# Kernel optimization log

Measured on AMD Instinct MI355X. Metric: run time of the kernel, lower is better.

The kernel has to match this reference:

```python
import jax, jax.numpy as jnp
import numpy as np

EMBED_DIM = 1024
NUM_HEADS = 16
HEAD_DIM = EMBED_DIM // NUM_HEADS


def setup_inputs() -> dict:
    key = jax.random.key(0)
    k_x, k_wqkv, k_bqkv, k_wo, k_bo = jax.random.split(key, 5)
    b, n = 2, 2048
    scale_in = 1.0 / np.sqrt(EMBED_DIM)
    return {
        "x": jax.random.normal(k_x, (b, n, EMBED_DIM), dtype=jnp.float32),
        "W_qkv": jax.random.normal(k_wqkv, (EMBED_DIM, 3 * EMBED_DIM), dtype=jnp.float32) * scale_in,
        "b_qkv": jnp.zeros((3 * EMBED_DIM,), dtype=jnp.float32),
        "W_out": jax.random.normal(k_wo, (EMBED_DIM, EMBED_DIM), dtype=jnp.float32) * scale_in,
        "b_out": jnp.zeros((EMBED_DIM,), dtype=jnp.float32),
    }


def _rope_rotate(t, cos, sin):
    # t: [b, h, n, hd]; cos/sin: [1, 1, n, hd//2]
    t1, t2 = jnp.split(t, 2, axis=-1)
    return jnp.concatenate([cos * t1 - sin * t2, sin * t1 + cos * t2], axis=-1)


def reference(x, W_qkv, b_qkv, W_out, b_out):
    b, n, d = x.shape
    h, hd = NUM_HEADS, HEAD_DIM

    qkv = x @ W_qkv + b_qkv                      # [b, n, 3d]
    q, k, v = jnp.split(qkv, 3, axis=-1)
    q, k, v = [t.reshape(b, n, h, hd).transpose(0, 2, 1, 3) for t in (q, k, v)]

    # RoPE tables
    hd2 = hd // 2
    theta = 10000.0 ** (-2.0 * jnp.arange(hd2, dtype=jnp.float32) / hd)
    freqs = jnp.arange(n, dtype=jnp.float32)[:, None] * theta[None, :]  # [n, hd2]
    cos = jnp.cos(freqs)[None, None]
    sin = jnp.sin(freqs)[None, None]
    q = _rope_rotate(q, cos, sin)
    k = _rope_rotate(k, cos, sin)

    scores = jnp.einsum('bhqd,bhkd->bhqk', q, k) / jnp.sqrt(jnp.float32(hd))
    attn = jax.nn.softmax(scores, axis=-1)       # [b, h, n, n]
    out = jnp.einsum('bhqk,bhkd->bhqd', attn, v)
    out = out.transpose(0, 2, 1, 3).reshape(b, n, d)
    return out @ W_out + b_out
```

## Files before the change

kernel.cpp:

```cpp
#include <hip/hip_runtime.h>
#include <hip/hip_bf16.h>
#include <math.h>

#define EMBED 1024
#define NHEAD 16
#define HD 64
#define BATCH 2
#define SEQ 2048
#define MTOT (BATCH * SEQ)
#define QKVN (3 * EMBED)

typedef __attribute__((ext_vector_type(8))) short short8;
typedef __attribute__((ext_vector_type(4))) float f32x4;

typedef __attribute__((address_space(1))) const unsigned int GUI;
typedef __attribute__((address_space(3))) unsigned int LUI;

__device__ __forceinline__ void gload_lds16(const void* src, void* dst) {
  __builtin_amdgcn_global_load_lds((GUI*)src, (LUI*)dst, 16, 0, 0);
}

__device__ __forceinline__ unsigned short f2bf(float f) {
  unsigned u = __builtin_bit_cast(unsigned, f);
  u += 0x7fffu + ((u >> 16) & 1u);
  return (unsigned short)(u >> 16);
}

__device__ __forceinline__ float bf2f(unsigned short u) {
  unsigned v = (unsigned)u << 16;
  return __builtin_bit_cast(float, v);
}

__device__ __forceinline__ unsigned cvt_pk_bf16(float lo, float hi) {
  unsigned r;
  asm("v_cvt_pk_bf16_f32 %0, %1, %2" : "=v"(r) : "v"(lo), "v"(hi));
  return r;
}

#if __has_builtin(__builtin_amdgcn_exp2f)
#define EXP2(x) __builtin_amdgcn_exp2f(x)
#else
#define EXP2(x) __builtin_exp2f(x)
#endif

#define QSCALE 0.1803368801111191f

__global__ __launch_bounds__(256) void k_prep(const float* __restrict__ x,
                                              unsigned short* __restrict__ Xb,
                                              const float* __restrict__ Wqkv,
                                              unsigned short* __restrict__ WqkvT,
                                              const float* __restrict__ Wout,
                                              unsigned short* __restrict__ WoT,
                                              float* __restrict__ cosT,
                                              float* __restrict__ sinT) {
  __shared__ float tile[32][33];
  const int bid = blockIdx.x, tid = threadIdx.x;
  if (bid < 4096) {
    int i = bid * 256 + tid;
    float4 v = reinterpret_cast<const float4*>(x)[i];
    ushort4 o;
    o.x = f2bf(v.x); o.y = f2bf(v.y); o.z = f2bf(v.z); o.w = f2bf(v.w);
    reinterpret_cast<ushort4*>(Xb)[i] = o;
  } else if (bid < 8192) {
    const float* W;
    unsigned short* WT;
    int n0, k0, Ncols;
    if (bid < 7168) {
      int idx = bid - 4096;
      W = Wqkv; WT = WqkvT; Ncols = QKVN;
      n0 = (idx % 96) * 32; k0 = (idx / 96) * 32;
    } else {
      int idx = bid - 7168;
      W = Wout; WT = WoT; Ncols = EMBED;
      n0 = (idx & 31) * 32; k0 = (idx >> 5) * 32;
    }
    const int tc = tid & 31, tr = tid >> 5;
    for (int i = 0; i < 4; i++) {
      int r = tr + i * 8;
      tile[r][tc] = W[(size_t)(k0 + r) * Ncols + n0 + tc];
    }
    __syncthreads();
    for (int i = 0; i < 4; i++) {
      int r = tr + i * 8;
      WT[(size_t)(n0 + r) * EMBED + k0 + tc] = f2bf(tile[tc][r]);
    }
  } else {
    int idx = (bid - 8192) * 256 + tid;
    if (idx < SEQ * 32) {
      int pos = idx >> 5, i = idx & 31;
      float theta = __expf((float)i * -0.28782313662425575f);
      float f = (float)pos * theta;
      cosT[idx] = cosf(f);
      sinT[idx] = sinf(f);
    }
  }
}

__device__ __forceinline__ void gemm_mainloop(const unsigned short* __restrict__ A,
                                              const unsigned short* __restrict__ Bt,
                                              unsigned short* Al, unsigned short* Bl,
                                              size_t m0, size_t n0,
                                              int tid, int l15, int g, int wm, int wn,
                                              f32x4 acc[4][4]) {
  const int w = tid >> 6;
  const int lane = tid & 63;
  const int srow = lane >> 3, slot = lane & 7;
  for (int k0 = 0; k0 < 1024; k0 += 64) {
    __syncthreads();
    for (int it = 0; it < 4; it++) {
      const int r = w * 32 + it * 8 + srow;
      const int sc = (slot ^ (r & 7)) * 8;
      gload_lds16(A + (m0 + r) * 1024 + k0 + sc, &Al[(w * 32 + it * 8) * 64]);
      gload_lds16(Bt + (n0 + r) * 1024 + k0 + sc, &Bl[(w * 32 + it * 8) * 64]);
    }
    __syncthreads();
    for (int kk = 0; kk < 2; kk++) {
      short8 fa[4], fb[4];
      const int xr = ((kk * 4 + g) ^ (l15 & 7)) * 8;
      for (int i = 0; i < 4; i++)
        fa[i] = *reinterpret_cast<const short8*>(&Al[(wm * 64 + i * 16 + l15) * 64 + xr]);
      for (int j = 0; j < 4; j++)
        fb[j] = *reinterpret_cast<const short8*>(&Bl[(wn * 64 + j * 16 + l15) * 64 + xr]);
      for (int i = 0; i < 4; i++)
        for (int j = 0; j < 4; j++)
          acc[i][j] = __builtin_amdgcn_mfma_f32_16x16x32_bf16(fa[i], fb[j], acc[i][j], 0, 0, 0);
    }
  }
}

__global__ __launch_bounds__(256) void k_qkv_gemm(const unsigned short* __restrict__ A,
                                                  const unsigned short* __restrict__ Bt,
                                                  const float* __restrict__ bias,
                                                  const float* __restrict__ cosT,
                                                  const float* __restrict__ sinT,
                                                  unsigned short* __restrict__ Qb,
                                                  unsigned short* __restrict__ Kb,
                                                  unsigned short* __restrict__ Vtg) {
  __shared__ alignas(16) unsigned short Al[128 * 64];
  __shared__ alignas(16) unsigned short Bl[128 * 64];
  const int tid = threadIdx.x;
  const int lane = tid & 63, l15 = lane & 15, g = lane >> 4;
  const int wid = tid >> 6, wm = wid >> 1, wn = wid & 1;
  const int bid = blockIdx.x;
  const int x = bid & 7, i6 = bid >> 3;
  const int nc = i6 >> 5, rr = i6 & 31;
  const int mp = x * 4 + (rr & 3);
  const int np = nc * 8 + (rr >> 2);
  const size_t m0 = (size_t)mp * 128;
  const size_t n0 = (size_t)np * 128;
  f32x4 acc[4][4] = {};
  gemm_mainloop(A, Bt, Al, Bl, m0, n0, tid, l15, g, wm, wn, acc);

  const int cbase = (int)n0 + wn * 64;
  const int sec = cbase >> 10;
  const int head = (cbase & 1023) >> 6;
  float bia[4];
  for (int j = 0; j < 4; j++) bia[j] = bias[cbase + j * 16 + l15];
  const size_t mw = m0 + wm * 64;

  if (sec == 2) {
    for (int i = 0; i < 4; i++) {
      size_t mbase = mw + i * 16 + g * 4;
      int bb = (int)(mbase >> 11), pos0 = (int)(mbase & 2047);
      int k0 = pos0 & 63;
      int col = (pos0 & ~63) | (k0 & 32) | (((k0 >> 2) & 3) << 3) | (((k0 >> 4) & 1) << 2);
      size_t hb = (size_t)(bb * NHEAD + head) * HD;
      for (int j = 0; j < 4; j++) {
        int d = j * 16 + l15;
        uint2 pk;
        pk.x = cvt_pk_bf16(acc[i][j][0] + bia[j], acc[i][j][1] + bia[j]);
        pk.y = cvt_pk_bf16(acc[i][j][2] + bia[j], acc[i][j][3] + bia[j]);
        *reinterpret_cast<uint2*>(Vtg + (hb + d) * SEQ + col) = pk;
      }
    }
  } else {
    unsigned short* dst = sec ? Kb : Qb;
    const float qs = sec ? 1.0f : QSCALE;
    for (int i = 0; i < 4; i++)
      for (int r = 0; r < 4; r++) {
        size_t m = mw + i * 16 + g * 4 + r;
        int bb = (int)(m >> 11), pos = (int)(m & 2047);
        size_t base = ((size_t)(bb * NHEAD + head) * SEQ + pos) * HD;
        const float* cr = cosT + pos * 32;
        const float* sr = sinT + pos * 32;
        for (int pl = 0; pl < 2; pl++) {
          int ii = pl * 16 + l15;
          float c = cr[ii], s = sr[ii];
          float lo = acc[i][pl][r] + bia[pl];
          float hi = acc[i][pl + 2][r] + bia[pl + 2];
          dst[base + ii]      = f2bf((c * lo - s * hi) * qs);
          dst[base + 32 + ii] = f2bf((s * lo + c * hi) * qs);
        }
      }
  }
}

__global__ __launch_bounds__(256) void k_out_gemm(const unsigned short* __restrict__ A,
                                                  const unsigned short* __restrict__ Bt,
                                                  const float* __restrict__ bias,
                                                  float* __restrict__ out) {
  __shared__ alignas(16) unsigned short Al[128 * 64];
  __shared__ alignas(16) unsigned short Bl[64 * 64];
  const int tid = threadIdx.x;
  const int lane = tid & 63, l15 = lane & 15, g = lane >> 4;
  const int wid = tid >> 6, wm = wid >> 1, wn = wid & 1;
  const int w = wid;
  const int srow = lane >> 3, slot = lane & 7;
  const int bid = blockIdx.x;
  const int tile = (bid & 7) * 64 + (bid >> 3);
  const size_t m0 = (size_t)(tile / 16) * 128;
  const size_t n0 = (size_t)(tile % 16) * 64;
  f32x4 acc[4][2] = {};

  for (int k0 = 0; k0 < 1024; k0 += 64) {
    __syncthreads();
    for (int it = 0; it < 4; it++) {
      const int r = w * 32 + it * 8 + srow;
      const int sc = (slot ^ (r & 7)) * 8;
      gload_lds16(A + (m0 + r) * 1024 + k0 + sc, &Al[(w * 32 + it * 8) * 64]);
    }
    for (int it = 0; it < 2; it++) {
      const int r = w * 16 + it * 8 + srow;
      const int sc = (slot ^ (r & 7)) * 8;
      gload_lds16(Bt + (n0 + r) * 1024 + k0 + sc, &Bl[(w * 16 + it * 8) * 64]);
    }
    __syncthreads();
    for (int kk = 0; kk < 2; kk++) {
      short8 fa[4], fb[2];
      const int xr = ((kk * 4 + g) ^ (l15 & 7)) * 8;
      for (int i = 0; i < 4; i++)
        fa[i] = *reinterpret_cast<const short8*>(&Al[(wm * 64 + i * 16 + l15) * 64 + xr]);
      for (int j = 0; j < 2; j++)
        fb[j] = *reinterpret_cast<const short8*>(&Bl[(wn * 32 + j * 16 + l15) * 64 + xr]);
      for (int i = 0; i < 4; i++)
        for (int j = 0; j < 2; j++)
          acc[i][j] = __builtin_amdgcn_mfma_f32_16x16x32_bf16(fa[i], fb[j], acc[i][j], 0, 0, 0);
    }
  }

  const int cbase = (int)n0 + wn * 32;
  const size_t mw = m0 + wm * 64;
  for (int i = 0; i < 4; i++)
    for (int r = 0; r < 4; r++) {
      size_t m = mw + i * 16 + g * 4 + r;
      for (int j = 0; j < 2; j++) {
        int col = cbase + j * 16 + l15;
        out[m * EMBED + col] = acc[i][j][r] + bias[col];
      }
    }
}

__global__ __launch_bounds__(256) void k_attn(const unsigned short* __restrict__ Q,
                                              const unsigned short* __restrict__ Kg,
                                              const unsigned short* __restrict__ Vtg,
                                              unsigned short* __restrict__ Opart,
                                              float* __restrict__ lpart) {
  __shared__ alignas(16) unsigned short Kt[2][64 * 64];
  __shared__ alignas(16) unsigned short Vt[2][64 * 64];
  const int tid = threadIdx.x, w = tid >> 6, lane = tid & 63;
  const int l15 = lane & 15, g = lane >> 4;
  const int srow = lane >> 3, slot = lane & 7;

  const int n = blockIdx.x;
  const int xcd = n & 7, m = n >> 3;
  const int qb = m & 15, z = m >> 4;
  const int sp = z & 1, bh = (z >> 1) * 8 + xcd;

  const unsigned short* Qp = Q + (size_t)bh * SEQ * HD;
  const unsigned short* Kp = Kg + (size_t)bh * SEQ * HD;
  const unsigned short* Vp = Vtg + (size_t)bh * HD * SEQ;
  const int q0 = qb * 128 + w * 32;

  short8 aq[2][2];
#pragma unroll
  for (int u = 0; u < 2; u++)
#pragma unroll
    for (int kk = 0; kk < 2; kk++)
      aq[u][kk] = *reinterpret_cast<const short8*>(
          Qp + (size_t)(q0 + u * 16 + l15) * HD + kk * 32 + g * 8);

  const int sr16 = w * 16 + srow;
  const int sc0 = (slot ^ (sr16 & 7)) * 8;
  const int kb0 = sp * 1024;

  const f32x4 z4 = {0.f, 0.f, 0.f, 0.f};
  f32x4 o[2][4] = {};
  float lrow[2] = {0.f, 0.f};

#define STAGE(tt, b)                                                             \
  do {                                                                           \
    const int kb_ = kb0 + (tt) * 64;                                             \
    gload_lds16(Kp + (size_t)(kb_ + sr16) * HD + sc0, &Kt[b][(w * 16) * 64]);    \
    gload_lds16(Vp + (size_t)sr16 * SEQ + kb_ + sc0, &Vt[b][(w * 16) * 64]);     \
    gload_lds16(Kp + (size_t)(kb_ + sr16 + 8) * HD + sc0,                        \
                &Kt[b][(w * 16 + 8) * 64]);                                      \
    gload_lds16(Vp + (size_t)(sr16 + 8) * SEQ + kb_ + sc0,                       \
                &Vt[b][(w * 16 + 8) * 64]);                                      \
  } while (0)

#define COMPUTE(cur)                                                             \
  do {                                                                           \
    const unsigned short* Ktc = Kt[cur];                                         \
    const unsigned short* Vtc = Vt[cur];                                         \
    f32x4 s[2][4];                                                               \
    {                                                                            \
      const int xr = (g ^ (l15 & 7)) * 8;                                        \
      _Pragma("unroll") for (int c = 0; c < 4; c++) {                            \
        short8 ak = *reinterpret_cast<const short8*>(&Ktc[(c * 16 + l15) * 64 + xr]); \
        s[0][c] = __builtin_amdgcn_mfma_f32_16x16x32_bf16(ak, aq[0][0], z4, 0, 0, 0); \
        s[1][c] = __builtin_amdgcn_mfma_f32_16x16x32_bf16(ak, aq[1][0], z4, 0, 0, 0); \
      }                                                                          \
    }                                                                            \
    {                                                                            \
      const int xr = ((4 + g) ^ (l15 & 7)) * 8;                                  \
      _Pragma("unroll") for (int c = 0; c < 4; c++) {                            \
        short8 ak = *reinterpret_cast<const short8*>(&Ktc[(c * 16 + l15) * 64 + xr]); \
        s[0][c] = __builtin_amdgcn_mfma_f32_16x16x32_bf16(ak, aq[0][1], s[0][c], 0, 0, 0); \
        s[1][c] = __builtin_amdgcn_mfma_f32_16x16x32_bf16(ak, aq[1][1], s[1][c], 0, 0, 0); \
      }                                                                          \
    }                                                                            \
    unsigned wpk[2][8];                                                          \
    _Pragma("unroll") for (int u = 0; u < 2; u++) {                              \
      float rs = 0.f;                                                            \
      _Pragma("unroll") for (int c = 0; c < 4; c++) {                            \
        float p0 = EXP2(s[u][c][0]);                                             \
        float p1 = EXP2(s[u][c][1]);                                             \
        float p2 = EXP2(s[u][c][2]);                                             \
        float p3 = EXP2(s[u][c][3]);                                             \
        rs += (p0 + p1) + (p2 + p3);                                             \
        wpk[u][2 * c]     = cvt_pk_bf16(p0, p1);                                 \
        wpk[u][2 * c + 1] = cvt_pk_bf16(p2, p3);                                 \
      }                                                                          \
      lrow[u] += rs;                                                             \
    }                                                                            \
    _Pragma("unroll") for (int kk = 0; kk < 2; kk++) {                           \
      const int xr = ((kk * 4 + g) ^ (l15 & 7)) * 8;                             \
      short8 pb0 = __builtin_bit_cast(short8,                                    \
          uint4{wpk[0][4 * kk], wpk[0][4 * kk + 1], wpk[0][4 * kk + 2], wpk[0][4 * kk + 3]}); \
      short8 pb1 = __builtin_bit_cast(short8,                                    \
          uint4{wpk[1][4 * kk], wpk[1][4 * kk + 1], wpk[1][4 * kk + 2], wpk[1][4 * kk + 3]}); \
      _Pragma("unroll") for (int c2 = 0; c2 < 4; c2++) {                         \
        short8 av = *reinterpret_cast<const short8*>(&Vtc[(c2 * 16 + l15) * 64 + xr]); \
        o[0][c2] = __builtin_amdgcn_mfma_f32_16x16x32_bf16(av, pb0, o[0][c2], 0, 0, 0); \
        o[1][c2] = __builtin_amdgcn_mfma_f32_16x16x32_bf16(av, pb1, o[1][c2], 0, 0, 0); \
      }                                                                          \
    }                                                                            \
  } while (0)

  STAGE(0, 0);

  for (int t = 0; t < 15; t++) {
    const int cur = t & 1;
    STAGE(t + 1, cur ^ 1);
    asm volatile("s_waitcnt vmcnt(4)" ::: "memory");
    __builtin_amdgcn_s_barrier();
    COMPUTE(cur);
    __builtin_amdgcn_s_barrier();
  }
  asm volatile("s_waitcnt vmcnt(0)" ::: "memory");
  __builtin_amdgcn_s_barrier();
  COMPUTE(1);

#undef STAGE
#undef COMPUTE

  const size_t ob = (size_t)(sp * 32 + bh) * SEQ * HD;
#pragma unroll
  for (int u = 0; u < 2; u++) {
    float l = lrow[u];
    l += __shfl_xor(l, 16, 64);
    l += __shfl_xor(l, 32, 64);
    const int pos = q0 + u * 16 + l15;
    if (g == 0) lpart[(size_t)(sp * 32 + bh) * SEQ + pos] = l;
    unsigned short* orow = Opart + ob + (size_t)pos * HD;
#pragma unroll
    for (int c2 = 0; c2 < 4; c2++) {
      uint2 pk;
      pk.x = cvt_pk_bf16(o[u][c2][0], o[u][c2][1]);
      pk.y = cvt_pk_bf16(o[u][c2][2], o[u][c2][3]);
      *reinterpret_cast<uint2*>(orow + c2 * 16 + g * 4) = pk;
    }
  }
}

__global__ __launch_bounds__(256) void k_merge(const unsigned short* __restrict__ Op,
                                               const float* __restrict__ lp,
                                               unsigned short* __restrict__ AO) {
  const int t = threadIdx.x;
  const int bh = blockIdx.x >> 5, pt = blockIdx.x & 31;
  const int pos = pt * 64 + (t >> 2), dc = (t & 3) * 16;
  const unsigned short* p0 = Op + ((size_t)bh * SEQ + pos) * HD + dc;
  const unsigned short* p1 = p0 + (size_t)32 * SEQ * HD;
  const float l = lp[(size_t)bh * SEQ + pos] + lp[(size_t)(32 + bh) * SEQ + pos];
  const float inv = 1.f / l;
  short8 a0 = *reinterpret_cast<const short8*>(p0);
  short8 a1 = *reinterpret_cast<const short8*>(p0 + 8);
  short8 b0 = *reinterpret_cast<const short8*>(p1);
  short8 b1 = *reinterpret_cast<const short8*>(p1 + 8);
  unsigned pk[8];
#pragma unroll
  for (int i = 0; i < 4; i++) {
    float s0 = bf2f((unsigned short)a0[2 * i])     + bf2f((unsigned short)b0[2 * i]);
    float s1 = bf2f((unsigned short)a0[2 * i + 1]) + bf2f((unsigned short)b0[2 * i + 1]);
    pk[i] = cvt_pk_bf16(s0 * inv, s1 * inv);
  }
#pragma unroll
  for (int i = 0; i < 4; i++) {
    float s0 = bf2f((unsigned short)a1[2 * i])     + bf2f((unsigned short)b1[2 * i]);
    float s1 = bf2f((unsigned short)a1[2 * i + 1]) + bf2f((unsigned short)b1[2 * i + 1]);
    pk[4 + i] = cvt_pk_bf16(s0 * inv, s1 * inv);
  }
  const int bb = bh >> 4, h = bh & 15;
  unsigned short* dst = AO + ((size_t)bb * SEQ + pos) * EMBED + h * HD + dc;
  *reinterpret_cast<uint4*>(dst)     = uint4{pk[0], pk[1], pk[2], pk[3]};
  *reinterpret_cast<uint4*>(dst + 8) = uint4{pk[4], pk[5], pk[6], pk[7]};
}

extern "C" void kernel_launch(void* const* d_in, const int* in_sizes, int n_in,
                              void* d_out, int out_size, void* d_ws, size_t ws_size,
                              hipStream_t stream) {
  const float* x    = (const float*)d_in[0];
  const float* Wqkv = (const float*)d_in[1];
  const float* bqkv = (const float*)d_in[2];
  const float* Wout = (const float*)d_in[3];
  const float* bout = (const float*)d_in[4];
  float* out = (float*)d_out;

  char* ws = (char*)d_ws;
  size_t off = 0;
  auto carve = [&](size_t bytes) {
    char* p = ws + off;
    off += (bytes + 255) & ~(size_t)255;
    return p;
  };
  float* cosT           = (float*)carve((size_t)SEQ * 32 * 4);
  float* sinT           = (float*)carve((size_t)SEQ * 32 * 4);
  unsigned short* Xb    = (unsigned short*)carve((size_t)MTOT * EMBED * 2);
  unsigned short* WqkvT = (unsigned short*)carve((size_t)QKVN * EMBED * 2);
  unsigned short* WoT   = (unsigned short*)carve((size_t)EMBED * EMBED * 2);
  unsigned short* Qb    = (unsigned short*)carve((size_t)MTOT * EMBED * 2);
  unsigned short* Kb    = (unsigned short*)carve((size_t)MTOT * EMBED * 2);
  unsigned short* Vtg   = (unsigned short*)carve((size_t)MTOT * EMBED * 2);
  unsigned short* AO    = (unsigned short*)carve((size_t)MTOT * EMBED * 2);
  unsigned short* Opart = (unsigned short*)carve((size_t)2 * 32 * SEQ * HD * 2);
  float* lpart          = (float*)carve((size_t)2 * 32 * SEQ * 4);

  k_prep<<<dim3(8448), 256, 0, stream>>>(x, Xb, Wqkv, WqkvT, Wout, WoT, cosT, sinT);
  k_qkv_gemm<<<dim3(768), 256, 0, stream>>>(Xb, WqkvT, bqkv, cosT, sinT, Qb, Kb, Vtg);
  k_attn<<<dim3(1024), 256, 0, stream>>>(Qb, Kb, Vtg, Opart, lpart);
  k_merge<<<dim3(1024), 256, 0, stream>>>(Opart, lpart, AO);
  k_out_gemm<<<dim3(512), 256, 0, stream>>>(AO, WoT, bout, out);
}
```

Measured before the change: 128.0 us.

## Fuse split-KV merge into output projection GEMM A-tile load

Removes the separate merge kernel by having the output GEMM read both partial attention outputs and row sums directly, combine and normalize them in registers, and write the merged bf16 tile into LDS. This drops one launch and the write and re-read of the intermediate attention-output buffer. In exchange the A-tile load becomes synchronous register loads plus ALU work instead of async global-to-LDS copies. Each element is also recomputed once per N-tile column block, so the merge work is repeated 16 times.

```diff
diff --git a/kernel.cpp b/kernel.cpp
--- a/kernel.cpp
+++ b/kernel.cpp
@@ -195,7 +195,8 @@
   }
 }
 
-__global__ __launch_bounds__(256) void k_out_gemm(const unsigned short* __restrict__ A,
+__global__ __launch_bounds__(256) void k_out_gemm(const unsigned short* __restrict__ Op,
+                                                  const float* __restrict__ lp,
                                                   const unsigned short* __restrict__ Bt,
                                                   const float* __restrict__ bias,
                                                   float* __restrict__ out) {
@@ -208,16 +209,36 @@
   const int srow = lane >> 3, slot = lane & 7;
   const int bid = blockIdx.x;
   const int tile = (bid & 7) * 64 + (bid >> 3);
-  const size_t m0 = (size_t)(tile / 16) * 128;
+  const int mp = tile / 16;
+  const size_t m0 = (size_t)mp * 128;
   const size_t n0 = (size_t)(tile % 16) * 64;
+  const int bb = mp >> 4;
+  const int posbase = (mp & 15) * 128;
+  const size_t slab = (size_t)32 * SEQ * HD;
   f32x4 acc[4][2] = {};
 
   for (int k0 = 0; k0 < 1024; k0 += 64) {
+    const int head = k0 >> 6;
+    const size_t bh = (size_t)(bb * NHEAD + head);
     __syncthreads();
     for (int it = 0; it < 4; it++) {
       const int r = w * 32 + it * 8 + srow;
-      const int sc = (slot ^ (r & 7)) * 8;
-      gload_lds16(A + (m0 + r) * 1024 + k0 + sc, &Al[(w * 32 + it * 8) * 64]);
+      const int pos = posbase + r;
+      const int gc = slot ^ (r & 7);
+      const unsigned short* p0 = Op + (bh * SEQ + pos) * HD + gc * 8;
+      short8 a = *reinterpret_cast<const short8*>(p0);
+      short8 b = *reinterpret_cast<const short8*>(p0 + slab);
+      const float l = lp[bh * SEQ + pos] + lp[(bh + 32) * SEQ + pos];
+      const float inv = 1.f / l;
+      unsigned pk[4];
+#pragma unroll
+      for (int i = 0; i < 4; i++) {
+        float s0 = bf2f((unsigned short)a[2 * i])     + bf2f((unsigned short)b[2 * i]);
+        float s1 = bf2f((unsigned short)a[2 * i + 1]) + bf2f((unsigned short)b[2 * i + 1]);
+        pk[i] = cvt_pk_bf16(s0 * inv, s1 * inv);
+      }
+      *reinterpret_cast<uint4*>(&Al[(size_t)r * 64 + slot * 8]) =
+          uint4{pk[0], pk[1], pk[2], pk[3]};
     }
     for (int it = 0; it < 2; it++) {
       const int r = w * 16 + it * 8 + srow;
@@ -383,39 +404,6 @@
   }
 }
 
-__global__ __launch_bounds__(256) void k_merge(const unsigned short* __restrict__ Op,
-                                               const float* __restrict__ lp,
-                                               unsigned short* __restrict__ AO) {
-  const int t = threadIdx.x;
-  const int bh = blockIdx.x >> 5, pt = blockIdx.x & 31;
-  const int pos = pt * 64 + (t >> 2), dc = (t & 3) * 16;
-  const unsigned short* p0 = Op + ((size_t)bh * SEQ + pos) * HD + dc;
-  const unsigned short* p1 = p0 + (size_t)32 * SEQ * HD;
-  const float l = lp[(size_t)bh * SEQ + pos] + lp[(size_t)(32 + bh) * SEQ + pos];
-  const float inv = 1.f / l;
-  short8 a0 = *reinterpret_cast<const short8*>(p0);
-  short8 a1 = *reinterpret_cast<const short8*>(p0 + 8);
-  short8 b0 = *reinterpret_cast<const short8*>(p1);
-  short8 b1 = *reinterpret_cast<const short8*>(p1 + 8);
-  unsigned pk[8];
-#pragma unroll
-  for (int i = 0; i < 4; i++) {
-    float s0 = bf2f((unsigned short)a0[2 * i])     + bf2f((unsigned short)b0[2 * i]);
-    float s1 = bf2f((unsigned short)a0[2 * i + 1]) + bf2f((unsigned short)b0[2 * i + 1]);
-    pk[i] = cvt_pk_bf16(s0 * inv, s1 * inv);
-  }
-#pragma unroll
-  for (int i = 0; i < 4; i++) {
-    float s0 = bf2f((unsigned short)a1[2 * i])     + bf2f((unsigned short)b1[2 * i]);
-    float s1 = bf2f((unsigned short)a1[2 * i + 1]) + bf2f((unsigned short)b1[2 * i + 1]);
-    pk[4 + i] = cvt_pk_bf16(s0 * inv, s1 * inv);
-  }
-  const int bb = bh >> 4, h = bh & 15;
-  unsigned short* dst = AO + ((size_t)bb * SEQ + pos) * EMBED + h * HD + dc;
-  *reinterpret_cast<uint4*>(dst)     = uint4{pk[0], pk[1], pk[2], pk[3]};
-  *reinterpret_cast<uint4*>(dst + 8) = uint4{pk[4], pk[5], pk[6], pk[7]};
-}
-
 extern "C" void kernel_launch(void* const* d_in, const int* in_sizes, int n_in,
                               void* d_out, int out_size, void* d_ws, size_t ws_size,
                               hipStream_t stream) {
@@ -441,13 +429,11 @@
   unsigned short* Qb    = (unsigned short*)carve((size_t)MTOT * EMBED * 2);
   unsigned short* Kb    = (unsigned short*)carve((size_t)MTOT * EMBED * 2);
   unsigned short* Vtg   = (unsigned short*)carve((size_t)MTOT * EMBED * 2);
-  unsigned short* AO    = (unsigned short*)carve((size_t)MTOT * EMBED * 2);
   unsigned short* Opart = (unsigned short*)carve((size_t)2 * 32 * SEQ * HD * 2);
   float* lpart          = (float*)carve((size_t)2 * 32 * SEQ * 4);
 
   k_prep<<<dim3(8448), 256, 0, stream>>>(x, Xb, Wqkv, WqkvT, Wout, WoT, cosT, sinT);
   k_qkv_gemm<<<dim3(768), 256, 0, stream>>>(Xb, WqkvT, bqkv, cosT, sinT, Qb, Kb, Vtg);
   k_attn<<<dim3(1024), 256, 0, stream>>>(Qb, Kb, Vtg, Opart, lpart);
-  k_merge<<<dim3(1024), 256, 0, stream>>>(Opart, lpart, AO);
-  k_out_gemm<<<dim3(512), 256, 0, stream>>>(AO, WoT, bout, out);
-}
+  k_out_gemm<<<dim3(512), 256, 0, stream>>>(Opart, lpart, WoT, bout, out);
+}
```

Result: slower. 172.6 us (+34.8%).
